# Performance work log

Measured on AMD Instinct MI355X. Metric: run time of the kernel, lower is better.

## Reference

```python
import jax, jax.numpy as jnp
import numpy as np

N_NODES = 100000
N_EDGES = 3200000
IN_DIM, HID_DIM, OUT_DIM = 512, 32, 16


def spmm(rows, cols, vals, dense):
    # out[r] = sum_{e: rows[e]==r} vals[e] * dense[cols[e]]  == adj @ dense (COO)
    gathered = vals[:, None] * dense[cols]          # [E, D]
    return jax.ops.segment_sum(gathered, rows, num_segments=N_NODES)


def gcn_layer(x, adj_rows, adj_cols, adj_vals, W):
    support = x @ W                                  # dense mm [N, out]
    return spmm(adj_rows, adj_cols, adj_vals, support)


def setup_inputs() -> dict:
    key = jax.random.key(0)
    ks = jax.random.split(key, 8)
    x = jax.random.normal(ks[0], (N_NODES, IN_DIM), dtype=jnp.float32)
    adj_rows = jax.random.randint(ks[1], (N_EDGES,), 0, N_NODES, dtype=jnp.int32)
    adj_cols = jax.random.randint(ks[2], (N_EDGES,), 0, N_NODES, dtype=jnp.int32)
    adj_vals = jax.random.uniform(ks[3], (N_EDGES,), dtype=jnp.float32)
    W1 = jax.random.normal(ks[4], (IN_DIM, HID_DIM), dtype=jnp.float32)
    W2 = jax.random.normal(ks[5], (HID_DIM, OUT_DIM), dtype=jnp.float32)
    W3 = jax.random.normal(ks[6], (OUT_DIM, HID_DIM), dtype=jnp.float32)
    W4 = jax.random.normal(ks[7], (HID_DIM, IN_DIM), dtype=jnp.float32)
    return {"x": x, "adj_rows": adj_rows, "adj_cols": adj_cols,
            "adj_vals": adj_vals, "W1": W1, "W2": W2, "W3": W3, "W4": W4}


def reference(x, adj_rows, adj_cols, adj_vals, W1, W2, W3, W4):
    encoded1 = gcn_layer(x, adj_rows, adj_cols, adj_vals, W1)        # [N, 32]
    encoded2 = gcn_layer(encoded1, adj_rows, adj_cols, adj_vals, W2) # [N, 16]
    decoded1 = gcn_layer(encoded2, adj_rows, adj_cols, adj_vals, W3) # [N, 32]
    decoded2 = gcn_layer(decoded1, adj_rows, adj_cols, adj_vals, W4) # [N, 512]
    return (decoded2, encoded2)
```

## Files before the change

kernel.cpp:

```cpp
#include <hip/hip_runtime.h>
#include <hip/hip_bf16.h>


#define N_NODES 100000
#define N_EDGES 3200000
#define RPB_LOG 7
#define RPB (1 << RPB_LOG)
#define NB ((N_NODES + RPB - 1) / RPB)
#define CHUNK 16384
#define NCHUNK ((N_EDGES + CHUNK - 1) / CHUNK)
#define EPT (CHUNK / 512)

typedef __attribute__((ext_vector_type(4))) float f32x4;
typedef __attribute__((ext_vector_type(8))) short s16x8;
typedef __attribute__((ext_vector_type(4))) unsigned short u16x4;
typedef __attribute__((ext_vector_type(4))) int i32x4;

static __device__ inline s16x8 cvt8(const float4& lo, const float4& hi) {
  unsigned p0, p1, p2, p3;
  asm("v_cvt_pk_bf16_f32 %0, %1, %2" : "=v"(p0) : "v"(lo.x), "v"(lo.y));
  asm("v_cvt_pk_bf16_f32 %0, %1, %2" : "=v"(p1) : "v"(lo.z), "v"(lo.w));
  asm("v_cvt_pk_bf16_f32 %0, %1, %2" : "=v"(p2) : "v"(hi.x), "v"(hi.y));
  asm("v_cvt_pk_bf16_f32 %0, %1, %2" : "=v"(p3) : "v"(hi.z), "v"(hi.w));
  i32x4 pi = {(int)p0, (int)p1, (int)p2, (int)p3};
  return __builtin_bit_cast(s16x8, pi);
}

static __device__ inline unsigned pk2(float a, float b) {
  unsigned p;
  asm("v_cvt_pk_bf16_f32 %0, %1, %2" : "=v"(p) : "v"(a), "v"(b));
  return p;
}
static __device__ inline float b2f(unsigned short u) {
  return __uint_as_float(((unsigned)u) << 16);
}

__global__ __launch_bounds__(256) void wconv12_kernel(
    const float* __restrict__ W1, const float* __restrict__ W2,
    uint4* __restrict__ Wfrag) {
  int s = blockIdx.x * 256 + threadIdx.x;
  if (s >= 1024) return;
  int lane = s & 63, kt = s >> 6;
  int n = lane & 15;
  int kb = kt * 32 + (lane >> 4) * 8;
  unsigned p[4];
#pragma unroll
  for (int i = 0; i < 4; ++i) {
    float lo = 0.f, hi = 0.f;
#pragma unroll
    for (int m = 0; m < 32; ++m) {
      float w2 = W2[m * 16 + n];
      lo += W1[(kb + 2 * i) * 32 + m] * w2;
      hi += W1[(kb + 2 * i + 1) * 32 + m] * w2;
    }
    p[i] = pk2(lo, hi);
  }
  Wfrag[s] = make_uint4(p[0], p[1], p[2], p[3]);
}

__global__ __launch_bounds__(256) void mm1_kernel(
    const float* __restrict__ x, const uint4* __restrict__ Wfrag,
    unsigned short* __restrict__ out) {
  const int t = threadIdx.x;
  const int lane = t & 63;
  const int w = t >> 6;
  const int rbase = blockIdx.x * 128 + w * 32;
  const int lrow = lane & 15;
  const int kg = lane >> 4;

  int r0c = rbase + lrow;       if (r0c > N_NODES - 1) r0c = N_NODES - 1;
  int r1c = rbase + 16 + lrow;  if (r1c > N_NODES - 1) r1c = N_NODES - 1;
  const float* xp0 = x + (size_t)r0c * 512 + kg * 8;
  const float* xp1 = x + (size_t)r1c * 512 + kg * 8;
  const s16x8* Wf = (const s16x8*)Wfrag;

  f32x4 acc0 = {0.f, 0.f, 0.f, 0.f}, acc1 = {0.f, 0.f, 0.f, 0.f};

#pragma unroll 4
  for (int kt = 0; kt < 16; ++kt) {
    float4 a0lo = *(const float4*)(xp0 + kt * 32);
    float4 a0hi = *(const float4*)(xp0 + kt * 32 + 4);
    float4 a1lo = *(const float4*)(xp1 + kt * 32);
    float4 a1hi = *(const float4*)(xp1 + kt * 32 + 4);
    s16x8 b = Wf[kt * 64 + lane];
    s16x8 a0 = cvt8(a0lo, a0hi);
    s16x8 a1 = cvt8(a1lo, a1hi);
    acc0 = __builtin_amdgcn_mfma_f32_16x16x32_bf16(a0, b, acc0, 0, 0, 0);
    acc1 = __builtin_amdgcn_mfma_f32_16x16x32_bf16(a1, b, acc1, 0, 0, 0);
  }

  const int col = lane & 15;
#pragma unroll
  for (int reg = 0; reg < 4; ++reg) {
    int r0 = rbase + kg * 4 + reg;
    if (r0 < N_NODES)
      out[(size_t)r0 * 16 + col] = (unsigned short)(pk2(acc0[reg], acc0[reg]) & 0xFFFF);
    int r1 = rbase + 16 + kg * 4 + reg;
    if (r1 < N_NODES)
      out[(size_t)r1 * 16 + col] = (unsigned short)(pk2(acc1[reg], acc1[reg]) & 0xFFFF);
  }
}

__global__ __launch_bounds__(512) void localsort_kernel(
    const int* __restrict__ rows, const int* __restrict__ cols,
    const float* __restrict__ vals, int2* __restrict__ cv_loc,
    int* __restrict__ ofs, int* __restrict__ gcnt) {
  __shared__ int lcnt[NB];
  __shared__ int lofs[NB + 1];
  __shared__ int ssum[512];
  const int c = blockIdx.x, t = threadIdx.x;
  const int c0 = c * CHUNK, c1 = min(c0 + CHUNK, N_EDGES);

  for (int i = t; i < NB; i += 512) lcnt[i] = 0;
  __syncthreads();

  int rr[EPT];
#pragma unroll
  for (int u = 0; u < EPT; ++u) {
    int e = c0 + t + u * 512;
    rr[u] = (e < c1) ? rows[e] : -1;
    if (rr[u] >= 0) atomicAdd(&lcnt[rr[u] >> RPB_LOG], 1);
  }
  __syncthreads();

  int v0 = (2 * t < NB) ? lcnt[2 * t] : 0;
  int v1 = (2 * t + 1 < NB) ? lcnt[2 * t + 1] : 0;
  if (v0) atomicAdd(&gcnt[2 * t], v0);
  if (v1) atomicAdd(&gcnt[2 * t + 1], v1);
  ssum[t] = v0 + v1;
  __syncthreads();
  for (int off = 1; off < 512; off <<= 1) {
    int xv = (t >= off) ? ssum[t - off] : 0;
    __syncthreads();
    ssum[t] += xv;
    __syncthreads();
  }
  int excl = (t == 0) ? 0 : ssum[t - 1];
  if (2 * t < NB) lofs[2 * t] = excl;
  if (2 * t + 1 < NB) lofs[2 * t + 1] = excl + v0;
  if (t == 511) lofs[NB] = ssum[511];
  __syncthreads();

  for (int i = t; i <= NB; i += 512) ofs[c * (NB + 1) + i] = lofs[i];
  for (int i = t; i < NB; i += 512) lcnt[i] = 0;
  __syncthreads();

#pragma unroll
  for (int u = 0; u < EPT; ++u) {
    int r = rr[u];
    if (r >= 0) {
      int e = c0 + t + u * 512;
      int b = r >> RPB_LOG;
      int rank = atomicAdd(&lcnt[b], 1);
      cv_loc[c0 + lofs[b] + rank] =
          make_int2(((r & (RPB - 1)) << 17) | cols[e], __float_as_int(vals[e]));
    }
  }
}

__global__ __launch_bounds__(1024) void scan782_kernel(
    const int* __restrict__ gcnt, int* __restrict__ bstart,
    int* __restrict__ row_ptr) {
  __shared__ int s[1024];
  int t = threadIdx.x;
  int v = (t < NB) ? gcnt[t] : 0;
  s[t] = v;
  __syncthreads();
  for (int off = 1; off < 1024; off <<= 1) {
    int xv = (t >= off) ? s[t - off] : 0;
    __syncthreads();
    s[t] += xv;
    __syncthreads();
  }
  if (t < NB) bstart[t] = s[t] - v;
  if (t == 0) { bstart[NB] = N_EDGES; row_ptr[N_NODES] = N_EDGES; }
}

__global__ __launch_bounds__(256) void refine3_kernel(
    const int* __restrict__ ofs, const int* __restrict__ bstart,
    const int2* __restrict__ cv_loc, unsigned* __restrict__ cv_csr,
    int* __restrict__ row_ptr) {
  __shared__ int gs[NCHUNK];
  __shared__ int sq[256];
  __shared__ int rcnt[RPB];
  __shared__ int rbase[RPB];
  const int b = blockIdx.x, t = threadIdx.x;

  int cnt_t = 0;
  if (t < NCHUNK) {
    int g0 = ofs[t * (NB + 1) + b];
    int g1 = ofs[t * (NB + 1) + b + 1];
    gs[t] = t * CHUNK + g0;
    cnt_t = g1 - g0;
  }
  if (t < RPB) rcnt[t] = 0;
  __syncthreads();

  for (int i = 0; i < cnt_t; ++i) {
    int2 e = cv_loc[gs[t] + i];
    atomicAdd(&rcnt[e.x >> 17], 1);
  }
  __syncthreads();

  int rv = (t < RPB) ? rcnt[t] : 0;
  sq[t] = rv;
  __syncthreads();
  for (int off = 1; off < RPB; off <<= 1) {
    int v = (t >= off && t < RPB) ? sq[t - off] : 0;
    __syncthreads();
    if (t < RPB) sq[t] += v;
    __syncthreads();
  }
  if (t < RPB) {
    int base = bstart[b] + sq[t] - rv;
    rbase[t] = base;
    int gr = (b << RPB_LOG) + t;
    if (gr < N_NODES) row_ptr[gr] = base;
    rcnt[t] = 0;
  }
  __syncthreads();

  for (int i = 0; i < cnt_t; ++i) {
    int2 e = cv_loc[gs[t] + i];
    int rl = e.x >> 17;
    int rank = atomicAdd(&rcnt[rl], 1);
    float v = __int_as_float(e.y);
    unsigned vb = pk2(v, v);
    cv_csr[rbase[rl] + rank] =
        ((unsigned)(e.x & 0x1FFFF) << 15) | (vb & 0x7FFF);
  }
}

template <int OM>
__global__ __launch_bounds__(256) void spmm_b16_kernel(
    const int* __restrict__ rp, const unsigned* __restrict__ colval,
    const unsigned short* __restrict__ in, unsigned short* __restrict__ outb,
    float* __restrict__ outf) {
  const int t = threadIdx.x;
  const int r = blockIdx.x * 64 + (t >> 2);
  const int q = t & 3;
  if (r >= N_NODES) return;
  const int k0 = rp[r], k1 = rp[r + 1];
  float a0 = 0.f, a1 = 0.f, a2 = 0.f, a3 = 0.f;

  int k = k0;
  for (; k + 7 < k1; k += 8) {
    unsigned cv[8];
#pragma unroll
    for (int u = 0; u < 8; ++u) cv[u] = colval[k + u];
    u16x4 g[8];
#pragma unroll
    for (int u = 0; u < 8; ++u)
      g[u] = *(const u16x4*)(in + (size_t)(cv[u] >> 15) * 16 + q * 4);
#pragma unroll
    for (int u = 0; u < 8; ++u) {
      float v = __uint_as_float((cv[u] & 0x7FFF) << 16);
      a0 += v * b2f(g[u][0]);
      a1 += v * b2f(g[u][1]);
      a2 += v * b2f(g[u][2]);
      a3 += v * b2f(g[u][3]);
    }
  }
  for (; k + 1 < k1; k += 2) {
    unsigned ca = colval[k], cb = colval[k + 1];
    u16x4 ga = *(const u16x4*)(in + (size_t)(ca >> 15) * 16 + q * 4);
    u16x4 gb = *(const u16x4*)(in + (size_t)(cb >> 15) * 16 + q * 4);
    float va = __uint_as_float((ca & 0x7FFF) << 16);
    float vb = __uint_as_float((cb & 0x7FFF) << 16);
    a0 += va * b2f(ga[0]); a1 += va * b2f(ga[1]);
    a2 += va * b2f(ga[2]); a3 += va * b2f(ga[3]);
    a0 += vb * b2f(gb[0]); a1 += vb * b2f(gb[1]);
    a2 += vb * b2f(gb[2]); a3 += vb * b2f(gb[3]);
  }
  if (k < k1) {
    unsigned cv = colval[k];
    u16x4 g = *(const u16x4*)(in + (size_t)(cv >> 15) * 16 + q * 4);
    float v = __uint_as_float((cv & 0x7FFF) << 16);
    a0 += v * b2f(g[0]); a1 += v * b2f(g[1]);
    a2 += v * b2f(g[2]); a3 += v * b2f(g[3]);
  }

  if (OM == 0 || OM == 1) {
    uint2 pk = make_uint2(pk2(a0, a1), pk2(a2, a3));
    *(uint2*)(outb + (size_t)r * 16 + q * 4) = pk;
  }
  if (OM == 1 || OM == 2) {
    *(float4*)(outf + (size_t)r * 16 + q * 4) = make_float4(a0, a1, a2, a3);
  }
}

__global__ __launch_bounds__(512) void mm4_kernel(
    const float* __restrict__ t3, const float* __restrict__ W3,
    const float* __restrict__ W4, float* __restrict__ out,
    int rows_per_block) {
  const int j = threadIdx.x;
  float w4c[32];
#pragma unroll
  for (int m = 0; m < 32; ++m) w4c[m] = W4[m * 512 + j];
  float w[16];
#pragma unroll
  for (int k = 0; k < 16; ++k) {
    float acc = 0.f;
#pragma unroll
    for (int m = 0; m < 32; ++m) acc += W3[k * 32 + m] * w4c[m];
    w[k] = acc;
  }
  int r0 = blockIdx.x * rows_per_block;
  int r1 = r0 + rows_per_block;
  if (r1 > N_NODES) r1 = N_NODES;
  for (int r = r0; r < r1; ++r) {
    const float* srow = t3 + (size_t)r * 16;
    float a0 = 0.f, a1 = 0.f, a2 = 0.f, a3 = 0.f;
#pragma unroll
    for (int k = 0; k < 16; k += 4) {
      a0 += srow[k + 0] * w[k + 0];
      a1 += srow[k + 1] * w[k + 1];
      a2 += srow[k + 2] * w[k + 2];
      a3 += srow[k + 3] * w[k + 3];
    }
    out[(size_t)r * 512 + j] = (a0 + a1) + (a2 + a3);
  }
}

extern "C" void kernel_launch(void* const* d_in, const int* in_sizes, int n_in,
                              void* d_out, int out_size, void* d_ws, size_t ws_size,
                              hipStream_t stream) {
  const float* x     = (const float*)d_in[0];
  const int*   arows = (const int*)d_in[1];
  const int*   acols = (const int*)d_in[2];
  const float* avals = (const float*)d_in[3];
  const float* W1    = (const float*)d_in[4];
  const float* W2    = (const float*)d_in[5];
  const float* W3    = (const float*)d_in[6];
  const float* W4    = (const float*)d_in[7];

  float* out = (float*)d_out;
  float* dec = out;
  float* enc = out + (size_t)N_NODES * 512;

  unsigned short* bh  = (unsigned short*)d_ws;
  unsigned short* bu  = bh + (size_t)N_NODES * 16;
  unsigned short* be  = bu + (size_t)N_NODES * 16;
  unsigned short* bt2 = be + (size_t)N_NODES * 16;
  float*          t3  = (float*)(bt2 + (size_t)N_NODES * 16);

  int2*     cv_loc  = (int2*)dec;
  unsigned* cv_csr  = (unsigned*)(cv_loc + N_EDGES);
  uint4*    Wfrag   = (uint4*)(cv_csr + N_EDGES);
  int*      ofs     = (int*)(Wfrag + 1024);
  int*      row_ptr = ofs + NCHUNK * (NB + 1);
  int*      bstart  = row_ptr + N_NODES + 1;
  int*      gcnt    = bstart + NB + 1;

  hipMemsetAsync(gcnt, 0, NB * sizeof(int), stream);
  wconv12_kernel<<<4, 256, 0, stream>>>(W1, W2, Wfrag);
  localsort_kernel<<<NCHUNK, 512, 0, stream>>>(arows, acols, avals, cv_loc, ofs, gcnt);
  scan782_kernel<<<1, 1024, 0, stream>>>(gcnt, bstart, row_ptr);
  refine3_kernel<<<NB, 256, 0, stream>>>(ofs, bstart, cv_loc, cv_csr, row_ptr);

  const int spGrid = (N_NODES + 63) / 64;
  mm1_kernel<<<(N_NODES + 127) / 128, 256, 0, stream>>>(x, Wfrag, bh);
  spmm_b16_kernel<0><<<spGrid, 256, 0, stream>>>(row_ptr, cv_csr, bh, bu, nullptr);
  spmm_b16_kernel<1><<<spGrid, 256, 0, stream>>>(row_ptr, cv_csr, bu, be, enc);
  spmm_b16_kernel<0><<<spGrid, 256, 0, stream>>>(row_ptr, cv_csr, be, bt2, nullptr);
  spmm_b16_kernel<2><<<spGrid, 256, 0, stream>>>(row_ptr, cv_csr, bt2, nullptr, t3);
  mm4_kernel<<<(N_NODES + 63) / 64, 512, 0, stream>>>(t3, W3, W4, dec, 64);
}
```

Baseline: 408.2 us.

## Fuse last SpMM with decoder matmul and balance refine edge distribution

The final SpMM is fused with the W3·W4 projection: each block aggregates 64 rows into shared memory and then writes the 512-wide decoded rows directly. This removes the fp32 t3 intermediate and the separate mm4 launch. The refine kernel now prefix-scans per-chunk counts so all 256 threads share edges evenly, where before each thread walked its own chunk serially. Buffers are relocated so cv_csr and row_ptr live in workspace and are not clobbered by the dec output, and the fused kernel unrolls its gathers by 8 for more memory-level parallelism.

```diff
diff --git a/kernel.cpp b/kernel.cpp
--- a/kernel.cpp
+++ b/kernel.cpp
@@ -176,11 +176,12 @@
   if (t == 0) { bstart[NB] = N_EDGES; row_ptr[N_NODES] = N_EDGES; }
 }
 
-__global__ __launch_bounds__(256) void refine3_kernel(
+__global__ __launch_bounds__(256) void refine4_kernel(
     const int* __restrict__ ofs, const int* __restrict__ bstart,
     const int2* __restrict__ cv_loc, unsigned* __restrict__ cv_csr,
     int* __restrict__ row_ptr) {
   __shared__ int gs[NCHUNK];
+  __shared__ int q[NCHUNK + 1];
   __shared__ int sq[256];
   __shared__ int rcnt[RPB];
   __shared__ int rbase[RPB];
@@ -193,11 +194,24 @@
     gs[t] = t * CHUNK + g0;
     cnt_t = g1 - g0;
   }
+  sq[t] = cnt_t;
+  __syncthreads();
+  for (int off = 1; off < 256; off <<= 1) {
+    int v = (t >= off) ? sq[t - off] : 0;
+    __syncthreads();
+    sq[t] += v;
+    __syncthreads();
+  }
+  if (t < NCHUNK) q[t] = sq[t] - cnt_t;
+  if (t == 0) q[NCHUNK] = sq[255];
   if (t < RPB) rcnt[t] = 0;
   __syncthreads();
-
-  for (int i = 0; i < cnt_t; ++i) {
-    int2 e = cv_loc[gs[t] + i];
+  const int Q = q[NCHUNK];
+
+  int lo = 0;
+  for (int i = t; i < Q; i += 256) {
+    while (q[lo + 1] <= i) ++lo;
+    int2 e = cv_loc[gs[lo] + (i - q[lo])];
     atomicAdd(&rcnt[e.x >> 17], 1);
   }
   __syncthreads();
@@ -220,8 +234,10 @@
   }
   __syncthreads();
 
-  for (int i = 0; i < cnt_t; ++i) {
-    int2 e = cv_loc[gs[t] + i];
+  lo = 0;
+  for (int i = t; i < Q; i += 256) {
+    while (q[lo + 1] <= i) ++lo;
+    int2 e = cv_loc[gs[lo] + (i - q[lo])];
     int rl = e.x >> 17;
     int rank = atomicAdd(&rcnt[rl], 1);
     float v = __int_as_float(e.y);
@@ -280,45 +296,96 @@
     a2 += v * b2f(g[2]); a3 += v * b2f(g[3]);
   }
 
-  if (OM == 0 || OM == 1) {
-    uint2 pk = make_uint2(pk2(a0, a1), pk2(a2, a3));
-    *(uint2*)(outb + (size_t)r * 16 + q * 4) = pk;
-  }
-  if (OM == 1 || OM == 2) {
+  uint2 pk = make_uint2(pk2(a0, a1), pk2(a2, a3));
+  *(uint2*)(outb + (size_t)r * 16 + q * 4) = pk;
+  if (OM == 1) {
     *(float4*)(outf + (size_t)r * 16 + q * 4) = make_float4(a0, a1, a2, a3);
   }
 }
 
-__global__ __launch_bounds__(512) void mm4_kernel(
-    const float* __restrict__ t3, const float* __restrict__ W3,
-    const float* __restrict__ W4, float* __restrict__ out,
-    int rows_per_block) {
-  const int j = threadIdx.x;
-  float w4c[32];
-#pragma unroll
-  for (int m = 0; m < 32; ++m) w4c[m] = W4[m * 512 + j];
-  float w[16];
-#pragma unroll
-  for (int k = 0; k < 16; ++k) {
-    float acc = 0.f;
-#pragma unroll
-    for (int m = 0; m < 32; ++m) acc += W3[k * 32 + m] * w4c[m];
-    w[k] = acc;
-  }
-  int r0 = blockIdx.x * rows_per_block;
-  int r1 = r0 + rows_per_block;
-  if (r1 > N_NODES) r1 = N_NODES;
-  for (int r = r0; r < r1; ++r) {
-    const float* srow = t3 + (size_t)r * 16;
-    float a0 = 0.f, a1 = 0.f, a2 = 0.f, a3 = 0.f;
-#pragma unroll
-    for (int k = 0; k < 16; k += 4) {
-      a0 += srow[k + 0] * w[k + 0];
-      a1 += srow[k + 1] * w[k + 1];
-      a2 += srow[k + 2] * w[k + 2];
-      a3 += srow[k + 3] * w[k + 3];
-    }
-    out[(size_t)r * 512 + j] = (a0 + a1) + (a2 + a3);
+__global__ __launch_bounds__(256) void spmm_dec_kernel(
+    const int* __restrict__ rp, const unsigned* __restrict__ colval,
+    const unsigned short* __restrict__ in, const float* __restrict__ W3,
+    const float* __restrict__ W4, float* __restrict__ out) {
+  __shared__ float t3s[64][20];
+  const int t = threadIdx.x;
+  const int r0 = blockIdx.x * 64;
+  const int lr = t >> 2;
+  const int q = t & 3;
+  const int r = r0 + lr;
+
+  float w4a[32], w4b[32];
+#pragma unroll
+  for (int m = 0; m < 32; ++m) {
+    w4a[m] = W4[m * 512 + t];
+    w4b[m] = W4[m * 512 + t + 256];
+  }
+  float wa[16], wb[16];
+#pragma unroll
+  for (int kk = 0; kk < 16; ++kk) {
+    float sa = 0.f, sb = 0.f;
+#pragma unroll
+    for (int m = 0; m < 32; ++m) {
+      float w3 = W3[kk * 32 + m];
+      sa += w3 * w4a[m];
+      sb += w3 * w4b[m];
+    }
+    wa[kk] = sa;
+    wb[kk] = sb;
+  }
+
+  float a0 = 0.f, a1 = 0.f, a2 = 0.f, a3 = 0.f;
+  if (r < N_NODES) {
+    const int k0 = rp[r], k1 = rp[r + 1];
+    int k = k0;
+    for (; k + 7 < k1; k += 8) {
+      unsigned cv[8];
+#pragma unroll
+      for (int u = 0; u < 8; ++u) cv[u] = colval[k + u];
+      u16x4 g[8];
+#pragma unroll
+      for (int u = 0; u < 8; ++u)
+        g[u] = *(const u16x4*)(in + (size_t)(cv[u] >> 15) * 16 + q * 4);
+#pragma unroll
+      for (int u = 0; u < 8; ++u) {
+        float v = __uint_as_float((cv[u] & 0x7FFF) << 16);
+        a0 += v * b2f(g[u][0]);
+        a1 += v * b2f(g[u][1]);
+        a2 += v * b2f(g[u][2]);
+        a3 += v * b2f(g[u][3]);
+      }
+    }
+    for (; k < k1; ++k) {
+      unsigned cv = colval[k];
+      u16x4 g = *(const u16x4*)(in + (size_t)(cv >> 15) * 16 + q * 4);
+      float v = __uint_as_float((cv & 0x7FFF) << 16);
+      a0 += v * b2f(g[0]); a1 += v * b2f(g[1]);
+      a2 += v * b2f(g[2]); a3 += v * b2f(g[3]);
+    }
+  }
+  t3s[lr][q * 4 + 0] = a0;
+  t3s[lr][q * 4 + 1] = a1;
+  t3s[lr][q * 4 + 2] = a2;
+  t3s[lr][q * 4 + 3] = a3;
+  __syncthreads();
+
+  const int nrows = min(64, N_NODES - r0);
+  for (int rr = 0; rr < nrows; ++rr) {
+    float4 c0 = *(const float4*)&t3s[rr][0];
+    float4 c1 = *(const float4*)&t3s[rr][4];
+    float4 c2 = *(const float4*)&t3s[rr][8];
+    float4 c3 = *(const float4*)&t3s[rr][12];
+    float sa = c0.x * wa[0] + c0.y * wa[1] + c0.z * wa[2] + c0.w * wa[3]
+             + c1.x * wa[4] + c1.y * wa[5] + c1.z * wa[6] + c1.w * wa[7]
+             + c2.x * wa[8] + c2.y * wa[9] + c2.z * wa[10] + c2.w * wa[11]
+             + c3.x * wa[12] + c3.y * wa[13] + c3.z * wa[14] + c3.w * wa[15];
+    float sb = c0.x * wb[0] + c0.y * wb[1] + c0.z * wb[2] + c0.w * wb[3]
+             + c1.x * wb[4] + c1.y * wb[5] + c1.z * wb[6] + c1.w * wb[7]
+             + c2.x * wb[8] + c2.y * wb[9] + c2.z * wb[10] + c2.w * wb[11]
+             + c3.x * wb[12] + c3.y * wb[13] + c3.z * wb[14] + c3.w * wb[15];
+    float* o = out + (size_t)(r0 + rr) * 512;
+    o[t] = sa;
+    o[t + 256] = sb;
   }
 }
 
@@ -341,28 +408,25 @@
   unsigned short* bh  = (unsigned short*)d_ws;
   unsigned short* bu  = bh + (size_t)N_NODES * 16;
   unsigned short* be  = bu + (size_t)N_NODES * 16;
-  unsigned short* bt2 = be + (size_t)N_NODES * 16;
-  float*          t3  = (float*)(bt2 + (size_t)N_NODES * 16);
-
-  int2*     cv_loc  = (int2*)dec;
-  unsigned* cv_csr  = (unsigned*)(cv_loc + N_EDGES);
-  uint4*    Wfrag   = (uint4*)(cv_csr + N_EDGES);
-  int*      ofs     = (int*)(Wfrag + 1024);
-  int*      row_ptr = ofs + NCHUNK * (NB + 1);
-  int*      bstart  = row_ptr + N_NODES + 1;
-  int*      gcnt    = bstart + NB + 1;
+  unsigned* cv_csr  = (unsigned*)(be + (size_t)N_NODES * 16);
+  int*      row_ptr = (int*)(cv_csr + N_EDGES);
+
+  int2*  cv_loc = (int2*)dec;
+  uint4* Wfrag  = (uint4*)(cv_loc + N_EDGES);
+  int*   ofs    = (int*)(Wfrag + 1024);
+  int*   bstart = ofs + NCHUNK * (NB + 1);
+  int*   gcnt   = bstart + NB + 1;
 
   hipMemsetAsync(gcnt, 0, NB * sizeof(int), stream);
   wconv12_kernel<<<4, 256, 0, stream>>>(W1, W2, Wfrag);
   localsort_kernel<<<NCHUNK, 512, 0, stream>>>(arows, acols, avals, cv_loc, ofs, gcnt);
   scan782_kernel<<<1, 1024, 0, stream>>>(gcnt, bstart, row_ptr);
-  refine3_kernel<<<NB, 256, 0, stream>>>(ofs, bstart, cv_loc, cv_csr, row_ptr);
+  refine4_kernel<<<NB, 256, 0, stream>>>(ofs, bstart, cv_loc, cv_csr, row_ptr);
 
   const int spGrid = (N_NODES + 63) / 64;
   mm1_kernel<<<(N_NODES + 127) / 128, 256, 0, stream>>>(x, Wfrag, bh);
   spmm_b16_kernel<0><<<spGrid, 256, 0, stream>>>(row_ptr, cv_csr, bh, bu, nullptr);
   spmm_b16_kernel<1><<<spGrid, 256, 0, stream>>>(row_ptr, cv_csr, bu, be, enc);
-  spmm_b16_kernel<0><<<spGrid, 256, 0, stream>>>(row_ptr, cv_csr, be, bt2, nullptr);
-  spmm_b16_kernel<2><<<spGrid, 256, 0, stream>>>(row_ptr, cv_csr, bt2, nullptr, t3);
-  mm4_kernel<<<(N_NODES + 63) / 64, 512, 0, stream>>>(t3, W3, W4, dec, 64);
-}
+  spmm_b16_kernel<0><<<spGrid, 256, 0, stream>>>(row_ptr, cv_csr, be, bh, nullptr);
+  spmm_dec_kernel<<<spGrid, 256, 0, stream>>>(row_ptr, cv_csr, bh, W3, W4, dec);
+}
```

Result: faster. 372.2 us (-8.8%).
